# Performance work log

Hardware: AMD Instinct MI355X
Metric: run time of the kernel (lower is better)

## Reference

```python
import jax, jax.numpy as jnp
import numpy as np

DIM = 512
HEADS = 8
EPS = 1e-5


def layer_norm(x, g, b):
    mu = jnp.mean(x, axis=-1, keepdims=True)
    var = jnp.mean(jnp.square(x - mu), axis=-1, keepdims=True)
    return (x - mu) * jax.lax.rsqrt(var + EPS) * g + b


def setup_inputs() -> dict:
    key = jax.random.key(0)
    ks = jax.random.split(key, 8)
    d = DIM
    s = 0.02
    return {
        "x": jax.random.normal(ks[0], (2, d, 64, 64), jnp.float32),
        "ln1_g": jnp.ones((d,), jnp.float32),
        "ln1_b": jnp.zeros((d,), jnp.float32),
        "w_qkv": jax.random.normal(ks[1], (d, 3 * d), jnp.float32) * s,
        "b_qkv": jnp.zeros((3 * d,), jnp.float32),
        "w_proj": jax.random.normal(ks[2], (d, d), jnp.float32) * s,
        "b_proj": jnp.zeros((d,), jnp.float32),
        "ln2_g": jnp.ones((d,), jnp.float32),
        "ln2_b": jnp.zeros((d,), jnp.float32),
        "w_ffn1": jax.random.normal(ks[3], (d, 4 * d), jnp.float32) * s,
        "b_ffn1": jnp.zeros((4 * d,), jnp.float32),
        "w_ffn2": jax.random.normal(ks[4], (4 * d, d), jnp.float32) * s,
        "b_ffn2": jnp.zeros((d,), jnp.float32),
    }


def reference(x, ln1_g, ln1_b, w_qkv, b_qkv, w_proj, b_proj,
              ln2_g, ln2_b, w_ffn1, b_ffn1, w_ffn2, b_ffn2):
    B, C, H, W = x.shape
    hd = C // HEADS
    x_in = x
    t = x.reshape(B, C, H * W).transpose(0, 2, 1)  # [B, N, C]
    h = layer_norm(t, ln1_g, ln1_b)
    qkv = h @ w_qkv + b_qkv  # [B, N, 3C]
    q, k, v = jnp.split(qkv, 3, axis=-1)
    def to_heads(a):
        return a.reshape(B, -1, HEADS, hd).transpose(0, 2, 1, 3)  # [B, h, N, hd]
    q, k, v = to_heads(q), to_heads(k), to_heads(v)
    # NOTE: module scales by 1/sqrt(C), not 1/sqrt(head_dim)
    attn = jnp.einsum('bhqd,bhkd->bhqk', q, k) / jnp.sqrt(jnp.float32(C))
    attn = jax.nn.softmax(attn, axis=-1)
    out = jnp.einsum('bhqk,bhkd->bhqd', attn, v)
    out = out.transpose(0, 2, 1, 3).reshape(B, -1, C)
    out = out @ w_proj + b_proj
    t = t + out
    h2 = layer_norm(t, ln2_g, ln2_b)
    ffn = jax.nn.relu(h2 @ w_ffn1 + b_ffn1) @ w_ffn2 + b_ffn2
    t = t + ffn
    y = t.transpose(0, 2, 1).reshape(B, C, H, W)
    return y + x_in
```

## Files before the change

kernel.cpp:

```cpp
#include <hip/hip_runtime.h>
#include <hip/hip_bf16.h>

typedef __bf16 bf16;
typedef __bf16 bf16x8 __attribute__((ext_vector_type(8)));
typedef __bf16 bf16x4 __attribute__((ext_vector_type(4)));
typedef __bf16 bf16x2 __attribute__((ext_vector_type(2)));
typedef float f32x4 __attribute__((ext_vector_type(4)));
typedef int int4v __attribute__((ext_vector_type(4)));
typedef int int2v __attribute__((ext_vector_type(2)));

#define DEV static __device__ __forceinline__

DEV void gload16(const void* g, void* l) {
    __builtin_amdgcn_global_load_lds(
        (const __attribute__((address_space(1))) void*)g,
        (__attribute__((address_space(3))) void*)l, 16, 0, 0);
}

DEV f32x4 mfma16(bf16x8 a, bf16x8 b, f32x4 c) {
    return __builtin_amdgcn_mfma_f32_16x16x32_bf16(a, b, c, 0, 0, 0);
}

DEV int cvtpk(float lo, float hi) {
    int r;
    asm("v_cvt_pk_bf16_f32 %0, %1, %2" : "=v"(r) : "v"(lo), "v"(hi));
    return r;
}

DEV float rexp2(float x) {
    float r;
    asm("v_exp_f32 %0, %1" : "=v"(r) : "v"(x));
    return r;
}

template <bool HASPO>
__global__ __launch_bounds__(512, 2)
void k_tln(const float* __restrict__ x, const bf16* __restrict__ po,
           const float* __restrict__ gg, const float* __restrict__ bb,
           bf16* __restrict__ h) {
    __shared__ char sm[HASPO ? 69632 : 35840];
    bf16* big = (bf16*)sm;
    float* red = (float*)(sm + 33536);
    float* mures = (float*)(sm + 35584);
    bf16* pob = (bf16*)(sm + 35840);

    int t = threadIdx.x;
    int bid = blockIdx.x;
    int nt = bid & 127, b = bid >> 7;
    int n0 = nt * 32;

    if (HASPO) {
        int rr = t >> 4, cs16 = t & 15;
        const bf16* ps = po + (size_t)(b * 4096 + n0 + rr) * 512 + cs16 * 32;
#pragma unroll
        for (int j = 0; j < 4; j++)
            *(bf16x8*)&pob[rr * 524 + cs16 * 32 + j * 8] =
                *(const bf16x8*)(ps + j * 8);
        __syncthreads();
    }

    int n = t & 31, cg = t >> 5;
    const float* xp = x + (size_t)b * 512 * 4096 +
                      (size_t)(cg * 32) * 4096 + n0 + n;
    float s = 0.f, ss = 0.f;
#pragma unroll
    for (int i = 0; i < 32; i++) {
        float v = xp[(size_t)i * 4096];
        if (HASPO) v += (float)pob[n * 524 + cg * 32 + i];
        s += v;
        ss += v * v;
        big[n * 524 + cg * 32 + i] = (bf16)v;
    }
    s += __shfl_xor(s, 32);
    ss += __shfl_xor(ss, 32);
    int w = t >> 6, l = t & 63;
    if (l < 32) {
        red[(w * 32 + n) * 2] = s;
        red[(w * 32 + n) * 2 + 1] = ss;
    }
    __syncthreads();
    if (t < 32) {
        float ts = 0.f, tss = 0.f;
#pragma unroll
        for (int ww = 0; ww < 8; ww++) {
            ts += red[(ww * 32 + t) * 2];
            tss += red[(ww * 32 + t) * 2 + 1];
        }
        float mu = ts * (1.f / 512.f);
        float var = tss * (1.f / 512.f) - mu * mu;
        mures[t * 2] = mu;
        mures[t * 2 + 1] = rsqrtf(var + 1e-5f);
    }
    __syncthreads();

    int nw = t >> 4, cs = t & 15;
    float mu = mures[nw * 2], rs = mures[nw * 2 + 1];
    bf16* hd = h + (size_t)(b * 4096 + n0 + nw) * 512;
#pragma unroll
    for (int j = 0; j < 4; j++) {
        int c = cs * 8 + j * 128;
        bf16x8 vv = *(const bf16x8*)&big[nw * 524 + c];
        f32x4 g0v = *(const f32x4*)(gg + c);
        f32x4 g1v = *(const f32x4*)(gg + c + 4);
        f32x4 b0v = *(const f32x4*)(bb + c);
        f32x4 b1v = *(const f32x4*)(bb + c + 4);
        bf16x8 o;
#pragma unroll
        for (int k = 0; k < 4; k++) {
            o[k] = (bf16)(((float)vv[k] - mu) * rs * g0v[k] + b0v[k]);
            o[k + 4] = (bf16)(((float)vv[k + 4] - mu) * rs * g1v[k] + b1v[k]);
        }
        *(bf16x8*)(hd + c) = o;
    }
}

__global__ __launch_bounds__(256)
void k_wtall(const float* __restrict__ w0, const float* __restrict__ w1,
             const float* __restrict__ w2, const float* __restrict__ w3,
             bf16* __restrict__ d0, bf16* __restrict__ d1,
             bf16* __restrict__ d2, bf16* __restrict__ d3) {
    __shared__ float tile[32][33];
    int bid = blockIdx.x;
    const float* w;
    bf16* d;
    int K, N, t;
    if (bid < 768)       { w = w0; d = d0; K = 512;  N = 1536; t = bid; }
    else if (bid < 1024) { w = w1; d = d1; K = 512;  N = 512;  t = bid - 768; }
    else if (bid < 2048) { w = w2; d = d2; K = 512;  N = 2048; t = bid - 1024; }
    else                 { w = w3; d = d3; K = 2048; N = 512;  t = bid - 2048; }
    int ntn = N >> 5;
    int kt = t / ntn, ntile = t % ntn;
    int k0 = kt * 32, n0 = ntile * 32;
    int tid = threadIdx.x;
    int nl = tid & 31, kl = tid >> 5;
#pragma unroll
    for (int i = 0; i < 4; i++) {
        int k = kl + i * 8;
        tile[k][nl] = w[(size_t)(k0 + k) * N + n0 + nl];
    }
    __syncthreads();
    int kl2 = tid & 31, nl2 = tid >> 5;
#pragma unroll
    for (int i = 0; i < 4; i++) {
        int n = nl2 + i * 8;
        d[(size_t)(n0 + n) * K + k0 + kl2] = (bf16)tile[kl2][n];
    }
}

template <int MODE, int BN>
__global__ __launch_bounds__(256, BN == 64 ? 3 : 2)
void k_gemm(const bf16* __restrict__ A, const bf16* __restrict__ BT,
            const float* __restrict__ bias, bf16* __restrict__ outb,
            bf16* __restrict__ vtout, const float* __restrict__ xin,
            const bf16* __restrict__ poin, float* __restrict__ yout,
            int M, int N, int K) {
    constexpr int CG = BN / 32;
    constexpr int BSZ = CG * 4096;
    __shared__ char smem[32768 + 2 * BSZ];
    int ntn = N / BN;
    int nwg = gridDim.x;
    int bid = blockIdx.x;
    int cpx = nwg >> 3;
    bid = (bid & 7) * cpx + (bid >> 3);
    int bm = bid / ntn, bn = bid % ntn;
    int m0 = bm * 128, n0 = bn * BN;
    int tid = threadIdx.x;
    int w = tid >> 6, l = tid & 63;
    int wm = w >> 1, wn = w & 1;
    int l15 = l & 15, lg = l >> 4;

    f32x4 acc[4][CG];
#pragma unroll
    for (int i = 0; i < 4; i++)
#pragma unroll
        for (int j = 0; j < CG; j++) acc[i][j] = (f32x4){0.f, 0.f, 0.f, 0.f};

    int srow = tid >> 3, sphys = tid & 7;
    int lrow_a = wm * 64 + l15;
    int lrow_b = wn * (BN / 2) + l15;

#define GEMM_STAGE(k0v, bb)                                                  \
    do {                                                                     \
        _Pragma("unroll") for (int s = 0; s < 4; s++) {                      \
            int row = s * 32 + srow;                                         \
            int k16 = sphys ^ (row & 7);                                     \
            gload16(A + (size_t)(m0 + row) * K + (k0v) + k16 * 8,            \
                    smem + (bb) * 16384 + s * 4096 + tid * 16);              \
        }                                                                    \
        _Pragma("unroll") for (int s = 0; s < CG; s++) {                     \
            int row = s * 32 + srow;                                         \
            int k16 = sphys ^ (row & 7);                                     \
            gload16(BT + (size_t)(n0 + row) * K + (k0v) + k16 * 8,           \
                    smem + 32768 + (bb) * BSZ + s * 4096 + tid * 16);        \
        }                                                                    \
    } while (0)

    int nk = K >> 6;
    GEMM_STAGE(0, 0);
    int cur = 0;
    for (int kt = 0; kt < nk; kt++) {
        if (kt + 1 < nk) {
            GEMM_STAGE((kt + 1) << 6, cur ^ 1);
            if constexpr (BN == 128)
                asm volatile("s_waitcnt vmcnt(8)" ::: "memory");
            else
                asm volatile("s_waitcnt vmcnt(6)" ::: "memory");
        } else {
            asm volatile("s_waitcnt vmcnt(0)" ::: "memory");
        }
        __builtin_amdgcn_s_barrier();
        __builtin_amdgcn_sched_barrier(0);
        const char* pA = smem + cur * 16384;
        const char* pB = smem + 32768 + cur * BSZ;
#pragma unroll
        for (int ks = 0; ks < 2; ks++) {
            bf16x8 af[4], bfr[CG];
#pragma unroll
            for (int rg = 0; rg < 4; rg++) {
                int row = lrow_a + rg * 16;
                af[rg] = *(const bf16x8*)(pA + row * 128 +
                                          (((lg + ks * 4) ^ (row & 7)) << 4));
            }
#pragma unroll
            for (int cg = 0; cg < CG; cg++) {
                int row = lrow_b + cg * 16;
                bfr[cg] = *(const bf16x8*)(pB + row * 128 +
                                           (((lg + ks * 4) ^ (row & 7)) << 4));
            }
#pragma unroll
            for (int rg = 0; rg < 4; rg++)
#pragma unroll
                for (int cg = 0; cg < CG; cg++)
                    acc[rg][cg] = mfma16(af[rg], bfr[cg], acc[rg][cg]);
        }
        __builtin_amdgcn_s_barrier();
        cur ^= 1;
    }
#undef GEMM_STAGE

    if constexpr (MODE == 2) {
        if (n0 >= 1024) {
            char* vl = smem;
#pragma unroll
            for (int cg = 0; cg < CG; cg++) {
                int col = wn * (BN / 2) + cg * 16 + l15;
                float bz = bias[n0 + col];
#pragma unroll
                for (int rg = 0; rg < 4; rg++) {
                    int rowb = wm * 64 + rg * 16 + lg * 4;
                    int2v qq = {cvtpk(acc[rg][cg][0] + bz, acc[rg][cg][1] + bz),
                                cvtpk(acc[rg][cg][2] + bz, acc[rg][cg][3] + bz)};
                    *(int2v*)(vl + col * 272 + rowb * 2) = qq;
                }
            }
            __syncthreads();
            int b = m0 >> 12, nrow0 = m0 & 4095;
            int dl = tid >> 3, c8 = tid & 7;
#pragma unroll
            for (int dd = 0; dd < BN / 32; dd++) {
                int d = dd * 32 + dl;
                int ch = (n0 - 1024) + d;
                bf16* dst = vtout +
                    ((size_t)((b * 8 + (ch >> 6)) * 64 + (ch & 63))) * 4096 + nrow0;
#pragma unroll
                for (int half = 0; half < 2; half++) {
                    int chunk = half * 8 + c8;
                    bf16x8 vv = *(const bf16x8*)(vl + d * 272 + chunk * 16);
                    *(bf16x8*)(dst + chunk * 8) = vv;
                }
            }
            return;
        }
    }

    if constexpr (MODE == 3) {
        float* ts = (float*)smem;
        int b = m0 >> 12, nrow0 = m0 & 4095;
#pragma unroll
        for (int cg = 0; cg < CG; cg++) {
            int lcol = wn * (BN / 2) + cg * 16 + l15;
            float bz = bias[n0 + lcol];
#pragma unroll
            for (int rg = 0; rg < 4; rg++) {
#pragma unroll
                for (int j = 0; j < 4; j++) {
                    int lrow = wm * 64 + rg * 16 + lg * 4 + j;
                    float v = acc[rg][cg][j] + bz +
                        (float)poin[(size_t)(m0 + lrow) * 512 + n0 + lcol];
                    ts[lcol * 132 + lrow] = v;
                }
            }
        }
        __syncthreads();
        int nl = (tid & 31) * 4, chh = tid >> 5;
#pragma unroll
        for (int q = 0; q < 8; q++) {
            int c = chh + q * 8;
            size_t off = ((size_t)b * 512 + n0 + c) * 4096 + nrow0 + nl;
            f32x4 xv = *(const f32x4*)(xin + off);
            f32x4 tv = *(const f32x4*)&ts[c * 132 + nl];
            f32x4 ov;
#pragma unroll
            for (int k2 = 0; k2 < 4; k2++) ov[k2] = 2.f * xv[k2] + tv[k2];
            *(f32x4*)(yout + off) = ov;
        }
        return;
    }

    constexpr int RS = BN * 2 + 8;
    constexpr int CH = BN / 8;
    char* ep = smem;
#pragma unroll
    for (int cg = 0; cg < CG; cg++) {
        int lcol = wn * (BN / 2) + cg * 16 + l15;
        float bz = bias[n0 + lcol];
#pragma unroll
        for (int rg = 0; rg < 4; rg++) {
#pragma unroll
            for (int j = 0; j < 4; j++) {
                int lrow = wm * 64 + rg * 16 + lg * 4 + j;
                float v = acc[rg][cg][j] + bz;
                if (MODE == 1) v = fmaxf(v, 0.f);
                *(bf16*)(ep + lrow * RS + lcol * 2) = (bf16)v;
            }
        }
    }
    __syncthreads();
    int cch = tid & (CH - 1);
    int rof = tid / CH;
    constexpr int RPP = 256 / CH;
#pragma unroll
    for (int i = 0; i < 128 / RPP; i++) {
        int row = i * RPP + rof;
        bf16x8 vv = *(const bf16x8*)(ep + row * RS + cch * 16);
        *(bf16x8*)(outb + (size_t)(m0 + row) * N + n0 + cch * 8) = vv;
    }
}

__global__ __launch_bounds__(256, 4)
void k_attn(const bf16* __restrict__ qkvb, const bf16* __restrict__ vt,
            bf16* __restrict__ attno) {
    __shared__ bf16 sK[2][64 * 64];
    __shared__ bf16 sV[2][64 * 64];
    const float sc = 0.044194173824159216f * 1.4426950408889634f;
    int bid = blockIdx.x;
    int nb = (bid & 7) * 128 + (bid >> 3);
    int bh = nb >> 6, qt = nb & 63;
    int b = bh >> 3, hh = bh & 7;
    int q0 = qt * 64;
    int tid = threadIdx.x, w = tid >> 6, l = tid & 63;
    int l15 = l & 15, lg = l >> 4, l7 = l15 & 7;
    int vperm = ((lg & 1) << 1) | (lg >> 1);
    const bf16* qbase = qkvb + (size_t)b * 4096 * 1536 + hh * 64;
    const bf16* kbase = qbase + 512;
    const bf16* vbase = vt + (size_t)bh * 64 * 4096;
    int srow = tid >> 3, sphys = tid & 7;

    const char* kp0 = (const char*)&sK[0][0] + l15 * 128 + ((lg ^ l7) << 4);
    const char* kp1 = (const char*)&sK[0][0] + l15 * 128 + (((4 + lg) ^ l7) << 4);
    const char* vp0 = (const char*)&sV[0][0] + l15 * 128 + ((vperm ^ l7) << 4);
    const char* vp1 = (const char*)&sV[0][0] + l15 * 128 + (((4 + vperm) ^ l7) << 4);
    char* dK0 = (char*)&sK[0][0] + tid * 16;
    char* dV0 = (char*)&sV[0][0] + tid * 16;
    const char* kg = (const char*)(kbase + srow * 1536 + (sphys ^ (srow & 7)) * 8);
    const char* vg = (const char*)(vbase + srow * 4096 + (sphys ^ (srow & 7)) * 8);

    gload16(kg, dK0);
    gload16(kg + 98304, dK0 + 4096);
    gload16(vg, dV0);
    gload16(vg + 262144, dV0 + 4096);
    kg += 196608;
    vg += 128;

    bf16x8 qf[2];
#pragma unroll
    for (int ks = 0; ks < 2; ks++) {
        bf16x8 v = *(const bf16x8*)(qbase +
            (size_t)(q0 + w * 16 + l15) * 1536 + ks * 32 + lg * 8);
        bf16x8 o;
#pragma unroll
        for (int j = 0; j < 8; j++) o[j] = (bf16)((float)v[j] * sc);
        qf[ks] = o;
    }
    bf16x8 ones;
#pragma unroll
    for (int j = 0; j < 8; j++) ones[j] = (bf16)1.0f;

    const f32x4 kZ = {0.f, 0.f, 0.f, 0.f};
    f32x4 accl = kZ;
    f32x4 acc[4];
#pragma unroll
    for (int df = 0; df < 4; df++) acc[df] = kZ;

#define ABODY(BUF, PF)                                                        \
    {                                                                         \
        if (PF) {                                                             \
            gload16(kg, dK0 + (1 - (BUF)) * 8192);                            \
            gload16(kg + 98304, dK0 + (1 - (BUF)) * 8192 + 4096);             \
            gload16(vg, dV0 + (1 - (BUF)) * 8192);                            \
            gload16(vg + 262144, dV0 + (1 - (BUF)) * 8192 + 4096);            \
            kg += 196608;                                                     \
            vg += 128;                                                        \
            asm volatile("s_waitcnt vmcnt(4)" ::: "memory");                  \
        } else {                                                              \
            asm volatile("s_waitcnt vmcnt(0)" ::: "memory");                  \
        }                                                                     \
        __builtin_amdgcn_s_barrier();                                         \
        __builtin_amdgcn_sched_barrier(0);                                    \
        f32x4 s0, s1, s2, s3;                                                 \
        __builtin_amdgcn_s_setprio(1);                                        \
        s0 = mfma16(*(const bf16x8*)(kp0 + (BUF) * 8192 + 0 * 2048), qf[0], kZ); \
        s0 = mfma16(*(const bf16x8*)(kp1 + (BUF) * 8192 + 0 * 2048), qf[1], s0); \
        s1 = mfma16(*(const bf16x8*)(kp0 + (BUF) * 8192 + 1 * 2048), qf[0], kZ); \
        s1 = mfma16(*(const bf16x8*)(kp1 + (BUF) * 8192 + 1 * 2048), qf[1], s1); \
        __builtin_amdgcn_s_setprio(0);                                        \
        float e0 = rexp2(s0[0]), e1 = rexp2(s0[1]);                           \
        float e2 = rexp2(s0[2]), e3 = rexp2(s0[3]);                           \
        float e4 = rexp2(s1[0]), e5 = rexp2(s1[1]);                           \
        float e6 = rexp2(s1[2]), e7 = rexp2(s1[3]);                           \
        __builtin_amdgcn_s_setprio(1);                                        \
        s2 = mfma16(*(const bf16x8*)(kp0 + (BUF) * 8192 + 2 * 2048), qf[0], kZ); \
        s2 = mfma16(*(const bf16x8*)(kp1 + (BUF) * 8192 + 2 * 2048), qf[1], s2); \
        s3 = mfma16(*(const bf16x8*)(kp0 + (BUF) * 8192 + 3 * 2048), qf[0], kZ); \
        s3 = mfma16(*(const bf16x8*)(kp1 + (BUF) * 8192 + 3 * 2048), qf[1], s3); \
        __builtin_amdgcn_s_setprio(0);                                        \
        int p0 = cvtpk(e0, e1), p1 = cvtpk(e2, e3);                           \
        int p2 = cvtpk(e4, e5), p3 = cvtpk(e6, e7);                           \
        asm("v_permlane16_swap_b32 %0, %1" : "+v"(p2), "+v"(p0));             \
        asm("v_permlane16_swap_b32 %0, %1" : "+v"(p3), "+v"(p1));             \
        {                                                                     \
            int4v ai = {p0, p1, p2, p3};                                      \
            bf16x8 af = __builtin_bit_cast(bf16x8, ai);                       \
            __builtin_amdgcn_s_setprio(1);                                    \
            acc[0] = mfma16(af, *(const bf16x8*)(vp0 + (BUF) * 8192 + 0 * 2048), acc[0]); \
            acc[1] = mfma16(af, *(const bf16x8*)(vp0 + (BUF) * 8192 + 1 * 2048), acc[1]); \
            acc[2] = mfma16(af, *(const bf16x8*)(vp0 + (BUF) * 8192 + 2 * 2048), acc[2]); \
            acc[3] = mfma16(af, *(const bf16x8*)(vp0 + (BUF) * 8192 + 3 * 2048), acc[3]); \
            accl = mfma16(af, ones, accl);                                    \
            __builtin_amdgcn_s_setprio(0);                                    \
        }                                                                     \
        float e8 = rexp2(s2[0]), e9 = rexp2(s2[1]);                           \
        float e10 = rexp2(s2[2]), e11 = rexp2(s2[3]);                         \
        float e12 = rexp2(s3[0]), e13 = rexp2(s3[1]);                         \
        float e14 = rexp2(s3[2]), e15 = rexp2(s3[3]);                         \
        int p4 = cvtpk(e8, e9), p5 = cvtpk(e10, e11);                         \
        int p6 = cvtpk(e12, e13), p7 = cvtpk(e14, e15);                       \
        asm("v_permlane16_swap_b32 %0, %1" : "+v"(p6), "+v"(p4));             \
        asm("v_permlane16_swap_b32 %0, %1" : "+v"(p7), "+v"(p5));             \
        {                                                                     \
            int4v ai = {p4, p5, p6, p7};                                      \
            bf16x8 af = __builtin_bit_cast(bf16x8, ai);                       \
            __builtin_amdgcn_s_setprio(1);                                    \
            acc[0] = mfma16(af, *(const bf16x8*)(vp1 + (BUF) * 8192 + 0 * 2048), acc[0]); \
            acc[1] = mfma16(af, *(const bf16x8*)(vp1 + (BUF) * 8192 + 1 * 2048), acc[1]); \
            acc[2] = mfma16(af, *(const bf16x8*)(vp1 + (BUF) * 8192 + 2 * 2048), acc[2]); \
            acc[3] = mfma16(af, *(const bf16x8*)(vp1 + (BUF) * 8192 + 3 * 2048), acc[3]); \
            accl = mfma16(af, ones, accl);                                    \
            __builtin_amdgcn_s_setprio(0);                                    \
        }                                                                     \
        __builtin_amdgcn_s_barrier();                                         \
    }

    for (int tt = 0; tt < 31; tt++) {
        ABODY(0, 1)
        ABODY(1, 1)
    }
    ABODY(0, 1)
    ABODY(1, 0)
#undef ABODY

    float invq[4];
#pragma unroll
    for (int j = 0; j < 4; j++) invq[j] = 1.0f / accl[j];

    bf16* ow = (bf16*)&sK[0][0] + w * 16 * 64;
#pragma unroll
    for (int df = 0; df < 4; df++) {
        int chunk = df * 2 + (l15 >> 3);
        int within = l15 & 7;
#pragma unroll
        for (int j = 0; j < 4; j++) {
            int q = lg * 4 + j;
            *(bf16*)((char*)ow + q * 128 + ((chunk ^ (q & 7)) << 4) + within * 2) =
                (bf16)(acc[df][j] * invq[j]);
        }
    }
    __syncthreads();
    const char* owr = (const char*)ow;
#pragma unroll
    for (int half = 0; half < 2; half++) {
        int r = l >> 2, ch = (l & 3) + half * 4;
        bf16x8 vv = *(const bf16x8*)(owr + r * 128 + ((ch ^ (r & 7)) << 4));
        *(bf16x8*)(attno + (size_t)(b * 4096 + q0 + w * 16 + r) * 512 +
                   hh * 64 + ch * 8) = vv;
    }
}

extern "C" void kernel_launch(void* const* d_in, const int* in_sizes, int n_in,
                              void* d_out, int out_size, void* d_ws, size_t ws_size,
                              hipStream_t stream) {
    const float* x = (const float*)d_in[0];
    const float* ln1g = (const float*)d_in[1];
    const float* ln1b = (const float*)d_in[2];
    const float* wqkv = (const float*)d_in[3];
    const float* bqkv = (const float*)d_in[4];
    const float* wproj = (const float*)d_in[5];
    const float* bproj = (const float*)d_in[6];
    const float* ln2g = (const float*)d_in[7];
    const float* ln2b = (const float*)d_in[8];
    const float* wffn1 = (const float*)d_in[9];
    const float* bffn1 = (const float*)d_in[10];
    const float* wffn2 = (const float*)d_in[11];
    const float* bffn2 = (const float*)d_in[12];
    float* y = (float*)d_out;

    char* ws = (char*)d_ws;
    bf16* po   = (bf16*)(ws + 0);
    bf16* h    = (bf16*)(ws + 16777216);
    bf16* qkvb = (bf16*)(ws + 25165824);
    bf16* vtb  = (bf16*)(ws + 50331648);
    bf16* f1   = (bf16*)(ws + 25165824);
    bf16* wqT  = (bf16*)(ws + 58720256);
    bf16* wpT  = (bf16*)(ws + 60293120);
    bf16* w1T  = (bf16*)(ws + 60817408);
    bf16* w2T  = (bf16*)(ws + 62914560);
    bf16* attno = h;

    k_tln<false><<<256, 512, 0, stream>>>(x, nullptr, ln1g, ln1b, h);
    k_wtall<<<3072, 256, 0, stream>>>(wqkv, wproj, wffn1, wffn2,
                                      wqT, wpT, w1T, w2T);
    k_gemm<2, 128><<<768, 256, 0, stream>>>(h, wqT, bqkv, qkvb, vtb,
                                            nullptr, nullptr, nullptr,
                                            8192, 1536, 512);
    k_attn<<<1024, 256, 0, stream>>>(qkvb, vtb, attno);
    k_gemm<0, 64><<<512, 256, 0, stream>>>(attno, wpT, bproj, po, nullptr,
                                           nullptr, nullptr, nullptr,
                                           8192, 512, 512);
    k_tln<true><<<256, 512, 0, stream>>>(x, po, ln2g, ln2b, h);
    k_gemm<1, 128><<<1024, 256, 0, stream>>>(h, w1T, bffn1, f1, nullptr,
                                             nullptr, nullptr, nullptr,
                                             8192, 2048, 512);
    k_gemm<3, 64><<<512, 256, 0, stream>>>(f1, w2T, bffn2, nullptr, nullptr,
                                           x, po, y, 8192, 512, 2048);
}
```

Baseline: 181.0 us.

## Add 256x256-tile 8-wave GEMM kernel for the FFN1 projection

Replaces the generic 128-tile GEMM for the FFN1 layer (8192x2048x512, ReLU) with a dedicated kernel. It uses 256x256 output tiles, 512 threads, 128KB of LDS, and a hand-scheduled double-buffered global_load_lds pipeline with explicit vmcnt waits, barriers and setprio around the MFMA bursts. The goal is more operand reuse per loaded byte and better overlap of loads with MFMAs. The cost is only 256 blocks, high register pressure from 32 accumulators per thread, and a two-pass epilogue through LDS. The ReLU is removed from the generic kernel's epilogue, which is now used only by the modes that do not need it.

```diff
diff --git a/kernel.cpp b/kernel.cpp
--- a/kernel.cpp
+++ b/kernel.cpp
@@ -320,7 +320,6 @@
             for (int j = 0; j < 4; j++) {
                 int lrow = wm * 64 + rg * 16 + lg * 4 + j;
                 float v = acc[rg][cg][j] + bz;
-                if (MODE == 1) v = fmaxf(v, 0.f);
                 *(bf16*)(ep + lrow * RS + lcol * 2) = (bf16)v;
             }
         }
@@ -334,6 +333,132 @@
         int row = i * RPP + rof;
         bf16x8 vv = *(const bf16x8*)(ep + row * RS + cch * 16);
         *(bf16x8*)(outb + (size_t)(m0 + row) * N + n0 + cch * 8) = vv;
+    }
+}
+
+__global__ __launch_bounds__(512, 2)
+void k_gemm8(const bf16* __restrict__ A, const bf16* __restrict__ BT,
+             const float* __restrict__ bias, bf16* __restrict__ outb) {
+    __shared__ char sL[131072];
+    int bid = blockIdx.x;
+    bid = (bid & 7) * 32 + (bid >> 3);
+    int bm = bid >> 3, bn = bid & 7;
+    int m0 = bm * 256, n0 = bn * 256;
+    int tid = threadIdx.x;
+    int w = tid >> 6, l = tid & 63;
+    int wm = w >> 2, wn = w & 3;
+    int l15 = l & 15, lg = l >> 4;
+    int cpr = (lg ^ ((l15 >> 1) & 3)) << 4;
+
+    f32x4 acc[8][4];
+#pragma unroll
+    for (int i = 0; i < 8; i++)
+#pragma unroll
+        for (int j = 0; j < 4; j++) acc[i][j] = (f32x4){0.f, 0.f, 0.f, 0.f};
+
+    int srow = tid >> 2, scp = tid & 3;
+    int kofs = (scp ^ ((srow >> 1) & 3)) * 8;
+    const bf16* gA0 = A + (size_t)(m0 + srow) * 512 + kofs;
+    const bf16* gA1 = gA0 + 128 * 512;
+    const bf16* gB0 = BT + (size_t)(n0 + srow) * 512 + kofs;
+    const bf16* gB1 = gB0 + 128 * 512;
+    char* dA = sL + tid * 16;
+    char* dB = sL + 65536 + tid * 16;
+    const char* pA0 = sL + (wm * 128 + l15) * 64 + cpr;
+    const char* pB0 = sL + 65536 + (wn * 64 + l15) * 64 + cpr;
+
+#define STGA(T, S, BUF)                                                       \
+    gload16(gA0 + (T) * 64 + (S) * 32, dA + (BUF) * 32768 + (S) * 16384);     \
+    gload16(gA1 + (T) * 64 + (S) * 32, dA + (BUF) * 32768 + (S) * 16384 + 8192);
+#define STGB(T, S, BUF)                                                       \
+    gload16(gB0 + (T) * 64 + (S) * 32, dB + (BUF) * 32768 + (S) * 16384);     \
+    gload16(gB1 + (T) * 64 + (S) * 32, dB + (BUF) * 32768 + (S) * 16384 + 8192);
+#define WB8 asm volatile("s_waitcnt vmcnt(8)" ::: "memory"); __builtin_amdgcn_s_barrier();
+#define WB4 asm volatile("s_waitcnt vmcnt(4)" ::: "memory"); __builtin_amdgcn_s_barrier();
+#define WB0 asm volatile("s_waitcnt vmcnt(0)" ::: "memory"); __builtin_amdgcn_s_barrier();
+#define WBN
+
+    bf16x8 bfr[4];
+
+#define PH(BUF, S, RGH, WAITC, STGC)                                          \
+    {                                                                         \
+        WAITC                                                                 \
+        if ((RGH) == 0) {                                                     \
+            _Pragma("unroll") for (int cg = 0; cg < 4; cg++)                  \
+                bfr[cg] = *(const bf16x8*)(pB0 + (BUF) * 32768 +              \
+                                           (S) * 16384 + cg * 1024);          \
+        }                                                                     \
+        bf16x8 af[4];                                                         \
+        _Pragma("unroll") for (int i = 0; i < 4; i++)                         \
+            af[i] = *(const bf16x8*)(pA0 + (BUF) * 32768 + (S) * 16384 +      \
+                                     ((RGH) * 4 + i) * 1024);                 \
+        STGC                                                                  \
+        __builtin_amdgcn_s_barrier();                                         \
+        asm volatile("s_waitcnt lgkmcnt(0)" ::: "memory");                    \
+        __builtin_amdgcn_sched_barrier(0);                                    \
+        __builtin_amdgcn_s_setprio(1);                                        \
+        _Pragma("unroll") for (int i = 0; i < 4; i++)                         \
+            _Pragma("unroll") for (int cg = 0; cg < 4; cg++)                  \
+                acc[(RGH) * 4 + i][cg] =                                      \
+                    mfma16(af[i], bfr[cg], acc[(RGH) * 4 + i][cg]);           \
+        __builtin_amdgcn_s_setprio(0);                                        \
+    }
+
+#define TILEF(T, BUF)                                                         \
+    PH(BUF, 0, 0, WB8, STGA(T + 1, 1, BUF ^ 1))                               \
+    PH(BUF, 0, 1, WBN, STGB(T + 1, 1, BUF ^ 1))                               \
+    PH(BUF, 1, 0, WB8, STGA(T + 2, 0, BUF))                                   \
+    PH(BUF, 1, 1, WBN, STGB(T + 2, 0, BUF))
+
+    STGA(0, 0, 0) STGB(0, 0, 0) STGA(0, 1, 0) STGB(0, 1, 0)
+    STGA(1, 0, 1) STGB(1, 0, 1)
+
+    TILEF(0, 0) TILEF(1, 1) TILEF(2, 0) TILEF(3, 1) TILEF(4, 0) TILEF(5, 1)
+    PH(0, 0, 0, WB8, STGA(7, 1, 1))
+    PH(0, 0, 1, WBN, STGB(7, 1, 1))
+    PH(0, 1, 0, WB8, )
+    PH(0, 1, 1, WBN, )
+    PH(1, 0, 0, WB4, )
+    PH(1, 0, 1, WBN, )
+    PH(1, 1, 0, WB0, )
+    PH(1, 1, 1, WBN, )
+#undef TILEF
+#undef PH
+#undef WB8
+#undef WB4
+#undef WB0
+#undef WBN
+#undef STGA
+#undef STGB
+
+    float bz[4];
+#pragma unroll
+    for (int cg = 0; cg < 4; cg++) bz[cg] = bias[n0 + wn * 64 + cg * 16 + l15];
+#pragma unroll
+    for (int h2 = 0; h2 < 2; h2++) {
+        __syncthreads();
+        if (wm == h2) {
+#pragma unroll
+            for (int rg = 0; rg < 8; rg++)
+#pragma unroll
+                for (int cg = 0; cg < 4; cg++)
+#pragma unroll
+                    for (int j = 0; j < 4; j++) {
+                        int rl = rg * 16 + lg * 4 + j;
+                        int cl = wn * 64 + cg * 16 + l15;
+                        float v = fmaxf(acc[rg][cg][j] + bz[cg], 0.f);
+                        *(bf16*)(sL + rl * 520 + cl * 2) = (bf16)v;
+                    }
+        }
+        __syncthreads();
+        int cch = tid & 31, rof = tid >> 5;
+#pragma unroll
+        for (int p = 0; p < 8; p++) {
+            int row = p * 16 + rof;
+            bf16x8 vv = *(const bf16x8*)(sL + row * 520 + cch * 16);
+            *(bf16x8*)(outb + (size_t)(m0 + h2 * 128 + row) * 2048 +
+                       n0 + cch * 8) = vv;
+        }
     }
 }
 
@@ -537,9 +662,7 @@
                                            nullptr, nullptr, nullptr,
                                            8192, 512, 512);
     k_tln<true><<<256, 512, 0, stream>>>(x, po, ln2g, ln2b, h);
-    k_gemm<1, 128><<<1024, 256, 0, stream>>>(h, w1T, bffn1, f1, nullptr,
-                                             nullptr, nullptr, nullptr,
-                                             8192, 2048, 512);
+    k_gemm8<<<256, 512, 0, stream>>>(h, w1T, bffn1, f1);
     k_gemm<3, 64><<<512, 256, 0, stream>>>(f1, w2T, bffn2, nullptr, nullptr,
                                            x, po, y, 8192, 512, 2048);
 }
```

New measurement: 179.1 us. No clear change (-1.1%).
